# Performance work log

Measured on AMD Instinct MI355X. Metric: run time of the kernel, lower is better.

## Reference

```python
import jax, jax.numpy as jnp
import numpy as np

VOCAB = 6; C_IN = 4; D = 256; L = 4; T = 4096; B = 2
EXPAND = 2; DI = EXPAND * D  # 512
DS = 16; DCONV = 4; DTR = 16  # dt_rank = ceil(D/16)


def setup_inputs() -> dict:
    key = jax.random.key(0)
    ks = jax.random.split(key, 16)
    rn = lambda k, shape, s=0.02: jax.random.normal(k, shape, jnp.float32) * s
    return {
        "seq": jax.random.randint(ks[0], (B, T), 0, VOCAB),
        "input": jax.random.normal(ks[1], (B, T, C_IN), jnp.float32),
        "emb_table": rn(ks[2], (VOCAB, D)),
        "inproj_w": rn(ks[3], (D, C_IN)),
        "inproj_b": jnp.zeros((D,), jnp.float32),
        "blk_in_w": rn(ks[4], (L, 2 * DI, D)),
        "blk_in_b": jnp.zeros((L, 2 * DI), jnp.float32),
        "conv_w": rn(ks[5], (L, DI, DCONV), 0.1),
        "conv_b": jnp.zeros((L, DI), jnp.float32),
        "xproj_w": rn(ks[6], (L, DTR + 2 * DS, DI)),
        "dt_w": rn(ks[7], (L, DI, DTR), 0.1),
        "dt_b": rn(ks[8], (L, DI), 0.1),
        "A_log": jnp.log(jnp.broadcast_to(jnp.arange(1, DS + 1, dtype=jnp.float32), (L, DI, DS))),
        "Dp": jnp.ones((L, DI), jnp.float32),
        "blk_out_w": rn(ks[9], (L, D, DI)),
        "blk_out_b": jnp.zeros((L, D), jnp.float32),
        "ln_g": jnp.ones((L, D), jnp.float32),
        "ln_b": jnp.zeros((L, D), jnp.float32),
        "head_w": rn(ks[10], (VOCAB, D)),
        "head_b": jnp.zeros((VOCAB,), jnp.float32),
        "outp_w": rn(ks[11], (C_IN, D)),
        "outp_b": jnp.zeros((C_IN,), jnp.float32),
    }


def _layernorm(x, g, b):
    mu = x.mean(-1, keepdims=True)
    var = ((x - mu) ** 2).mean(-1, keepdims=True)
    return (x - mu) * jax.lax.rsqrt(var + 1e-5) * g + b


def _mamba(x, in_w, in_b, cw, cb, xpw, dtw, dtb, alog, dparam, ow, ob):
    # x: (B, T, D). Standard mamba-ssm Mamba block (d_state=DS, d_conv=DCONV, expand=2).
    Bsz = x.shape[0]
    xz = x @ in_w.T + in_b                      # (B, T, 2*DI)
    xs, z = jnp.split(xz, 2, axis=-1)           # each (B, T, DI)
    # causal depthwise conv1d over time
    xt = jnp.pad(xs.transpose(0, 2, 1), ((0, 0), (0, 0), (DCONV - 1, 0)))  # (B, DI, T+3)
    xc = jax.lax.conv_general_dilated(xt, cw[:, None, :], (1,), 'VALID',
                                      feature_group_count=DI)             # (B, DI, T)
    xc = jax.nn.silu(xc + cb[None, :, None]).transpose(0, 2, 1)           # (B, T, DI)
    # input-dependent dt, B, C
    x_dbl = xc @ xpw.T                          # (B, T, DTR+2*DS)
    dt, Bm, Cm = jnp.split(x_dbl, [DTR, DTR + DS], axis=-1)
    dt = jax.nn.softplus(dt @ dtw.T + dtb)      # (B, T, DI)
    A = -jnp.exp(alog)                          # (DI, DS)
    dA = jnp.exp(dt[..., None] * A)                                  # (B, T, DI, DS)
    dBx = dt[..., None] * Bm[:, :, None, :] * xc[..., None]          # (B, T, DI, DS)

    def step(h, ins):
        dA_t, dBx_t, C_t = ins                  # (B,DI,DS), (B,DI,DS), (B,DS)
        h = dA_t * h + dBx_t
        return h, jnp.einsum('bds,bs->bd', h, C_t)

    h0 = jnp.zeros((Bsz, DI, DS), xc.dtype)
    _, ys = jax.lax.scan(step, h0, (dA.transpose(1, 0, 2, 3),
                                    dBx.transpose(1, 0, 2, 3),
                                    Cm.transpose(1, 0, 2)))
    y = ys.transpose(1, 0, 2) + dparam * xc     # (B, T, DI)
    y = y * jax.nn.silu(z)
    return y @ ow.T + ob                        # (B, T, D)


def reference(seq, input, emb_table, inproj_w, inproj_b, blk_in_w, blk_in_b,
              conv_w, conv_b, xproj_w, dt_w, dt_b, A_log, Dp,
              blk_out_w, blk_out_b, ln_g, ln_b, head_w, head_b, outp_w, outp_b):
    x = emb_table[seq] + input @ inproj_w.T + inproj_b   # (B, T, D)
    for l in range(L):
        mx = _mamba(x, blk_in_w[l], blk_in_b[l], conv_w[l], conv_b[l],
                    xproj_w[l], dt_w[l], dt_b[l], A_log[l], Dp[l],
                    blk_out_w[l], blk_out_b[l])
        x = _layernorm(x + mx, ln_g[l], ln_b[l])
    return (x @ head_w.T + head_b, x @ outp_w.T + outp_b)
```

## Files before the change

### kernel.cpp

```cpp
#include <hip/hip_runtime.h>

typedef unsigned short u16;
typedef unsigned int u32;
typedef short bf16x8 __attribute__((ext_vector_type(8)));
typedef float f32x4 __attribute__((ext_vector_type(4)));

#define Tlen 4096
#define NTOK 8192
#define NCH  128
#define CH   32

enum : int {
  OFF_EMB     = 16,
  OFF_INPUT   = OFF_EMB + 1536,
  OFF_INPROJW = OFF_INPUT + 32768,
  OFF_INPROJB = OFF_INPROJW + 1024,
  OFF_BLKINW  = OFF_INPROJB + 256,
  OFF_BLKINB  = OFF_BLKINW + 1048576,
  OFF_CONVW   = OFF_BLKINB + 4096,
  OFF_CONVB   = OFF_CONVW + 8192,
  OFF_XPROJW  = OFF_CONVB + 2048,
  OFF_DTW     = OFF_XPROJW + 98304,
  OFF_DTB     = OFF_DTW + 32768,
  OFF_A       = OFF_DTB + 2048,
  OFF_DP      = OFF_A + 32768,
  OFF_BLKOUTW = OFF_DP + 2048,
  OFF_BLKOUTB = OFF_BLKOUTW + 524288,
  OFF_LNG     = OFF_BLKOUTB + 1024,
  OFF_LNB     = OFF_LNG + 1024,
  OFF_HEADW   = OFF_LNB + 1024,
  OFF_HEADB   = OFF_HEADW + 1536,
  OFF_OUTPW   = OFF_HEADB + 16,
  OFF_OUTPB   = OFF_OUTPW + 1024,
  OFF_X       = OFF_OUTPB + 16,
  OFF_DT      = OFF_X + NTOK*256,
  OFF_SD      = OFF_DT + NTOK*512,
  OFF_BM      = OFF_SD + 131072,
  OFF_CM      = OFF_BM + 131072,
  OFF_XSBL    = OFF_CM + 131072,
  OFF_Z16     = OFF_XSBL + NTOK*256,
  OFF_XC16    = OFF_Z16 + NTOK*256,
  OFF_X16     = OFF_XC16 + NTOK*256,
  OFF_WIN16   = OFF_X16 + NTOK*128,
  OFF_WOUT16  = OFF_WIN16 + 524288,
  OFF_BXD16   = OFF_WOUT16 + 262144,
  OFF_TOT     = OFF_BXD16 + 557056,
};

__device__ inline float bf2f(u16 u) { return __uint_as_float(((u32)u) << 16); }
__device__ inline u16 f2bf(float f) {
  u32 x = __float_as_uint(f);
  u32 r = x + 0x7fffu + ((x >> 16) & 1u);
  return (u16)(r >> 16);
}

__global__ void k_sentinel(u32* dout, int nw) {
  int i = blockIdx.x * blockDim.x + threadIdx.x;
  if (i < nw) dout[i] = 0x46404640u;
}

__global__ void k_detect(const u16* emb, int n, int* flag) {
  __shared__ int bad;
  if (threadIdx.x == 0) bad = 0;
  __syncthreads();
  int local = 0;
  for (int i = threadIdx.x; i < n; i += blockDim.x) {
    float v = bf2f(emb[i]);
    if (!(fabsf(v) < 100.0f)) local = 1;
  }
  if (local) atomicOr(&bad, 1);
  __syncthreads();
  if (threadIdx.x == 0) flag[0] = bad ? 0 : 1;
}

struct Seg { const void* src; int n; int off; int op; };
struct ConvArgs { Seg seg[21]; int nseg; };

__global__ void k_convert(ConvArgs a, float* ws, const int* flag) {
  int isb = *flag;
  for (int sgi = 0; sgi < a.nseg; sgi++) {
    Seg sg = a.seg[sgi];
    for (int i = blockIdx.x * blockDim.x + threadIdx.x; i < sg.n;
         i += gridDim.x * blockDim.x) {
      float v;
      if (isb) v = bf2f(((const u16*)sg.src)[i]);
      else     v = ((const float*)sg.src)[i];
      if (sg.op) v = -__expf(v);
      ws[sg.off + i] = v;
    }
  }
}

__global__ void k_w16(float* ws) {
  u16* win = (u16*)(ws + OFF_WIN16);
  u16* wout = (u16*)(ws + OFF_WOUT16);
  for (int i = blockIdx.x * blockDim.x + threadIdx.x; i < 1048576 + 524288;
       i += gridDim.x * blockDim.x) {
    if (i < 1048576) win[i] = f2bf(ws[OFF_BLKINW + i]);
    else             wout[i - 1048576] = f2bf(ws[OFF_BLKOUTW + i - 1048576]);
  }
}

__global__ void k_weff(float* ws) {
  u16* bxd = (u16*)(ws + OFF_BXD16);
  const int NXD = 4 * 544 * 512;
  for (int idx = blockIdx.x * blockDim.x + threadIdx.x; idx < NXD;
       idx += gridDim.x * blockDim.x) {
    int l = idx / (544 * 512);
    int rem = idx - l * (544 * 512);
    int row = rem >> 9, k = rem & 511;
    const float* xpw = ws + OFF_XPROJW + l * 24576;
    float v;
    if (row < 32) {
      v = xpw[(16 + row) * 512 + k];
    } else {
      const float* dtw = ws + OFF_DTW + l * 8192 + (row - 32) * 16;
      v = 0.f;
      #pragma unroll
      for (int r = 0; r < 16; r++) v += dtw[r] * xpw[r * 512 + k];
    }
    bxd[idx] = f2bf(v);
  }
}

__global__ __launch_bounds__(256) void k_embed(const int* seq, float* ws) {
  int n = blockIdx.x, d = threadIdx.x;
  int s = seq[n];
  float4 iv = *(const float4*)(ws + OFF_INPUT + n * 4);
  float4 wv = *(const float4*)(ws + OFF_INPROJW + d * 4);
  float acc = ws[OFF_EMB + s * 256 + d] + ws[OFF_INPROJB + d]
            + iv.x * wv.x + iv.y * wv.y + iv.z * wv.z + iv.w * wv.w;
  ws[OFF_X + (size_t)n * 256 + d] = acc;
  ((u16*)(ws + OFF_X16))[(size_t)n * 256 + d] = f2bf(acc);
}

__global__ __launch_bounds__(256) void k_gemm_in(float* ws, int l) {
  __shared__ u16 As[128][40];
  __shared__ u16 Bs[128][40];
  __shared__ u16 ot[64][136];
  int m0 = blockIdx.x * 128, n0g = blockIdx.y * 128;
  int t = threadIdx.x;
  int w = t >> 6, lane = t & 63;
  int fr = lane & 15, fq = lane >> 4;
  int wr = (w >> 1) * 64, wc = (w & 1) * 64;
  const u16* Ab = (const u16*)(ws + OFF_X16);
  const u16* Bb = (const u16*)(ws + OFF_WIN16) + (size_t)l * 1024 * 256;
  const float* bias = ws + OFF_BLKINB + l * 1024;
  f32x4 acc[4][4] = {};
  for (int k0 = 0; k0 < 256; k0 += 32) {
    __syncthreads();
    #pragma unroll
    for (int cc = 0; cc < 2; cc++) {
      int c = t + cc * 256;
      int row = c >> 2, cg = (c & 3) * 8;
      *(uint4*)&As[row][cg] =
          *(const uint4*)(Ab + (size_t)(m0 + row) * 256 + k0 + cg);
      *(uint4*)&Bs[row][cg] =
          *(const uint4*)(Bb + (size_t)(n0g + row) * 256 + k0 + cg);
    }
    __syncthreads();
    bf16x8 af[4], bf_[4];
    #pragma unroll
    for (int f = 0; f < 4; f++) {
      af[f]  = *(const bf16x8*)&As[wr + f * 16 + fr][fq * 8];
      bf_[f] = *(const bf16x8*)&Bs[wc + f * 16 + fr][fq * 8];
    }
    #pragma unroll
    for (int i = 0; i < 4; i++)
      #pragma unroll
      for (int j = 0; j < 4; j++)
        acc[i][j] = __builtin_amdgcn_mfma_f32_16x16x32_bf16(af[i], bf_[j],
                                                            acc[i][j], 0, 0, 0);
  }
  u16* plane; int cb0;
  if (n0g < 512) { plane = (u16*)(ws + OFF_XSBL); cb0 = n0g; }
  else           { plane = (u16*)(ws + OFF_Z16);  cb0 = n0g - 512; }
  #pragma unroll
  for (int hh = 0; hh < 2; hh++) {
    __syncthreads();
    if ((w >> 1) == hh) {
      #pragma unroll
      for (int i = 0; i < 4; i++)
        #pragma unroll
        for (int j = 0; j < 4; j++) {
          int col = wc + j * 16 + fr;
          float bv = bias[n0g + col];
          #pragma unroll
          for (int r = 0; r < 4; r++)
            ot[i * 16 + fq * 4 + r][col] = f2bf(acc[i][j][r] + bv);
        }
    }
    __syncthreads();
    int row = t >> 2, c0 = (t & 3) * 32;
    uint4 q0 = *(const uint4*)&ot[row][c0];
    uint4 q1 = *(const uint4*)&ot[row][c0 + 8];
    uint4 q2 = *(const uint4*)&ot[row][c0 + 16];
    uint4 q3 = *(const uint4*)&ot[row][c0 + 24];
    u16* dst = plane + (size_t)(m0 + hh * 64 + row) * 512 + cb0 + c0;
    *(uint4*)(dst + 0) = q0;
    *(uint4*)(dst + 8) = q1;
    *(uint4*)(dst + 16) = q2;
    *(uint4*)(dst + 24) = q3;
  }
}

__global__ __launch_bounds__(512) void k_conv(float* ws, int l) {
  int n0 = blockIdx.x * 16;
  int d = threadIdx.x;
  const float* cw = ws + OFF_CONVW + l * 2048;
  float4 w4 = *(const float4*)(cw + d * 4);
  float cbv = ws[OFF_CONVB + l * 512 + d];
  const u16* xs16 = (const u16*)(ws + OFF_XSBL);
  u16* xc16 = (u16*)(ws + OFF_XC16);
  float xm3, xm2, xm1;
  if ((n0 & (Tlen - 1)) == 0) {
    xm3 = xm2 = xm1 = 0.f;
  } else {
    xm3 = bf2f(xs16[(size_t)(n0 - 3) * 512 + d]);
    xm2 = bf2f(xs16[(size_t)(n0 - 2) * 512 + d]);
    xm1 = bf2f(xs16[(size_t)(n0 - 1) * 512 + d]);
  }
  #pragma unroll
  for (int tok = 0; tok < 16; tok++) {
    int n = n0 + tok;
    float xc = bf2f(xs16[(size_t)n * 512 + d]);
    float acc = cbv + xm3 * w4.x + xm2 * w4.y + xm1 * w4.z + xc * w4.w;
    float sv = acc / (1.f + __expf(-acc));
    xc16[(size_t)n * 512 + d] = f2bf(sv);
    xm3 = xm2; xm2 = xm1; xm1 = xc;
  }
}

__global__ __launch_bounds__(256) void k_gemm_xd(float* ws, int l) {
  __shared__ u16 dts[64][136];
  int by = blockIdx.y;
  int m0 = blockIdx.x * 64;
  int w = threadIdx.x >> 6, lane = threadIdx.x & 63;
  const u16* Ab = (const u16*)(ws + OFF_XC16);
  const u16* Bb = (const u16*)(ws + OFF_BXD16) + (size_t)l * 544 * 512;
  int ak = (lane >> 4) * 8;
  const u16* ap = Ab + (size_t)(m0 + w * 16 + (lane & 15)) * 512 + ak;
  int rowbase = w * 16 + (lane >> 4) * 4;
  if (by < 8) {
    const u16* bp = Bb + (size_t)(32 + by * 64 + (lane & 15)) * 512 + ak;
    f32x4 acc[4] = {};
    bf16x8 a0 = *(const bf16x8*)ap;
    bf16x8 b0[4];
    #pragma unroll
    for (int j = 0; j < 4; j++) b0[j] = *(const bf16x8*)(bp + (size_t)j * 8192);
    #pragma unroll 2
    for (int k0 = 1; k0 < 16; k0++) {
      bf16x8 a1 = *(const bf16x8*)(ap + k0 * 32);
      bf16x8 b1[4];
      #pragma unroll
      for (int j = 0; j < 4; j++)
        b1[j] = *(const bf16x8*)(bp + (size_t)j * 8192 + k0 * 32);
      #pragma unroll
      for (int j = 0; j < 4; j++)
        acc[j] = __builtin_amdgcn_mfma_f32_16x16x32_bf16(a0, b0[j], acc[j], 0, 0, 0);
      a0 = a1;
      #pragma unroll
      for (int j = 0; j < 4; j++) b0[j] = b1[j];
    }
    #pragma unroll
    for (int j = 0; j < 4; j++)
      acc[j] = __builtin_amdgcn_mfma_f32_16x16x32_bf16(a0, b0[j], acc[j], 0, 0, 0);
    const float* dtb = ws + OFF_DTB + l * 512;
    #pragma unroll
    for (int j = 0; j < 4; j++) {
      float bv = dtb[by * 64 + j * 16 + (lane & 15)];
      #pragma unroll
      for (int r = 0; r < 4; r++) {
        float s = acc[j][r] + bv;
        float dtv = (s > 20.f) ? s : log1pf(__expf(s));
        dts[rowbase + r][j * 16 + (lane & 15)] = f2bf(dtv);
      }
    }
    __syncthreads();
    u16* dt16 = (u16*)(ws + OFF_DT);
    int tt = threadIdx.x;
    int row = tt >> 2, part = tt & 3;
    uint4 v0 = *(const uint4*)&dts[row][part * 16];
    uint4 v1 = *(const uint4*)&dts[row][part * 16 + 8];
    u16* dst = dt16 + (size_t)(m0 + row) * 512 + by * 64 + part * 16;
    *(uint4*)dst = v0;
    *(uint4*)(dst + 8) = v1;
  } else {
    const u16* bp = Bb + (size_t)(lane & 15) * 512 + ak;
    f32x4 acc[2] = {};
    bf16x8 a0 = *(const bf16x8*)ap;
    bf16x8 b0[2];
    #pragma unroll
    for (int j = 0; j < 2; j++) b0[j] = *(const bf16x8*)(bp + (size_t)j * 8192);
    #pragma unroll 2
    for (int k0 = 1; k0 < 16; k0++) {
      bf16x8 a1 = *(const bf16x8*)(ap + k0 * 32);
      bf16x8 b1[2];
      #pragma unroll
      for (int j = 0; j < 2; j++)
        b1[j] = *(const bf16x8*)(bp + (size_t)j * 8192 + k0 * 32);
      #pragma unroll
      for (int j = 0; j < 2; j++)
        acc[j] = __builtin_amdgcn_mfma_f32_16x16x32_bf16(a0, b0[j], acc[j], 0, 0, 0);
      a0 = a1;
      #pragma unroll
      for (int j = 0; j < 2; j++) b0[j] = b1[j];
    }
    #pragma unroll
    for (int j = 0; j < 2; j++)
      acc[j] = __builtin_amdgcn_mfma_f32_16x16x32_bf16(a0, b0[j], acc[j], 0, 0, 0);
    int c = lane & 15;
    #pragma unroll
    for (int r = 0; r < 4; r++) {
      ws[OFF_BM + (size_t)(m0 + rowbase + r) * 16 + c] = acc[0][r];
      ws[OFF_CM + (size_t)(m0 + rowbase + r) * 16 + c] = acc[1][r];
    }
  }
}

__global__ __launch_bounds__(512) void k_scan1(float* ws, int l) {
  __shared__ u16 dt_s[8][512];
  __shared__ u16 xc_s[8][512];
  __shared__ float Bls[CH * 16];
  int blk = blockIdx.x;
  int b = blk >> 7, ch = blk & 127;
  int d = threadIdx.x;
  int nbase = b * Tlen + ch * CH;
  Bls[d] = ws[OFF_BM + (size_t)nbase * 16 + d];
  const float* Ap = ws + OFF_A + l * 8192 + d * 16;
  float Ar[16];
  *(float4*)&Ar[0]  = *(const float4*)(Ap + 0);
  *(float4*)&Ar[4]  = *(const float4*)(Ap + 4);
  *(float4*)&Ar[8]  = *(const float4*)(Ap + 8);
  *(float4*)&Ar[12] = *(const float4*)(Ap + 12);
  float h[16];
  #pragma unroll
  for (int s = 0; s < 16; s++) h[s] = 0.f;
  float sumdt = 0.f;
  const u16* dtg = (const u16*)(ws + OFF_DT) + (size_t)nbase * 512;
  const u16* xcg = (const u16*)(ws + OFF_XC16) + (size_t)nbase * 512;
  int lr = d >> 6, lc = (d & 63) * 8;
  uint4 pd = *(const uint4*)(dtg + (size_t)lr * 512 + lc);
  uint4 px = *(const uint4*)(xcg + (size_t)lr * 512 + lc);
  for (int st = 0; st < 4; st++) {
    *(uint4*)&dt_s[lr][lc] = pd;
    *(uint4*)&xc_s[lr][lc] = px;
    if (st < 3) {
      pd = *(const uint4*)(dtg + (size_t)(st * 8 + 8 + lr) * 512 + lc);
      px = *(const uint4*)(xcg + (size_t)(st * 8 + 8 + lr) * 512 + lc);
    }
    __syncthreads();
    #pragma unroll
    for (int tk = 0; tk < 8; tk++) {
      int tt = st * 8 + tk;
      float dtv = bf2f(dt_s[tk][d]);
      float xv = bf2f(xc_s[tk][d]);
      sumdt += dtv;
      float dtx = dtv * xv;
      #pragma unroll
      for (int s = 0; s < 16; s++)
        h[s] = __expf(dtv * Ar[s]) * h[s] + dtx * Bls[tt * 16 + s];
    }
    __syncthreads();
  }
  ws[OFF_SD + (size_t)blk * 512 + d] = sumdt;
  float* bl = ws + OFF_XSBL + ((size_t)blk * 512 + d) * 16;
  *(float4*)(bl + 0)  = make_float4(h[0], h[1], h[2], h[3]);
  *(float4*)(bl + 4)  = make_float4(h[4], h[5], h[6], h[7]);
  *(float4*)(bl + 8)  = make_float4(h[8], h[9], h[10], h[11]);
  *(float4*)(bl + 12) = make_float4(h[12], h[13], h[14], h[15]);
}

__global__ __launch_bounds__(256) void k_scan2(float* ws, int l) {
  int q = blockIdx.x * 256 + threadIdx.x;
  int b = q >> 13, ds = q & 8191, d = ds >> 4;
  float Av = ws[OFF_A + l * 8192 + ds];
  float* blhs = ws + OFF_XSBL;
  const float* sdp = ws + OFF_SD;
  size_t base = (size_t)(b * NCH) * 8192 + ds;
  size_t sbase = (size_t)(b * NCH) * 512 + d;
  float blv[4], sd[4];
  #pragma unroll
  for (int k = 0; k < 4; k++) {
    blv[k] = blhs[base + (size_t)k * 8192];
    sd[k] = sdp[sbase + (size_t)k * 512];
  }
  float h = 0.f;
  for (int g = 0; g < 32; g++) {
    float nblv[4], nsd[4];
    if (g < 31) {
      #pragma unroll
      for (int k = 0; k < 4; k++) {
        nblv[k] = blhs[base + (size_t)(g * 4 + 4 + k) * 8192];
        nsd[k] = sdp[sbase + (size_t)(g * 4 + 4 + k) * 512];
      }
    }
    #pragma unroll
    for (int k = 0; k < 4; k++) {
      blhs[base + (size_t)(g * 4 + k) * 8192] = h;
      h = __expf(sd[k] * Av) * h + blv[k];
    }
    #pragma unroll
    for (int k = 0; k < 4; k++) { blv[k] = nblv[k]; sd[k] = nsd[k]; }
  }
}

__global__ __launch_bounds__(512) void k_scan3(float* ws, int l) {
  __shared__ u16 dt_s[8][512];
  __shared__ u16 xc_s[8][512];
  __shared__ u16 z_s[8][512];
  __shared__ u16 y_s[8][512];
  __shared__ float Bls[CH * 16];
  __shared__ float Cls[CH * 16];
  int blk = blockIdx.x;
  int b = blk >> 7, ch = blk & 127;
  int d = threadIdx.x;
  int nbase = b * Tlen + ch * CH;
  Bls[d] = ws[OFF_BM + (size_t)nbase * 16 + d];
  Cls[d] = ws[OFF_CM + (size_t)nbase * 16 + d];
  const float* Ap = ws + OFF_A + l * 8192 + d * 16;
  float Ar[16];
  *(float4*)&Ar[0]  = *(const float4*)(Ap + 0);
  *(float4*)&Ar[4]  = *(const float4*)(Ap + 4);
  *(float4*)&Ar[8]  = *(const float4*)(Ap + 8);
  *(float4*)&Ar[12] = *(const float4*)(Ap + 12);
  float Dv = ws[OFF_DP + l * 512 + d];
  const float* hs = ws + OFF_XSBL + ((size_t)blk * 512 + d) * 16;
  float h[16];
  *(float4*)&h[0]  = *(const float4*)(hs + 0);
  *(float4*)&h[4]  = *(const float4*)(hs + 4);
  *(float4*)&h[8]  = *(const float4*)(hs + 8);
  *(float4*)&h[12] = *(const float4*)(hs + 12);
  const u16* dtg = (const u16*)(ws + OFF_DT) + (size_t)nbase * 512;
  u16* xcg = (u16*)(ws + OFF_XC16) + (size_t)nbase * 512;
  const u16* zg = (const u16*)(ws + OFF_Z16) + (size_t)nbase * 512;
  int lr = d >> 6, lc = (d & 63) * 8;
  size_t off0 = (size_t)lr * 512 + lc;
  uint4 pd = *(const uint4*)(dtg + off0);
  uint4 px = *(const uint4*)(xcg + off0);
  uint4 pz = *(const uint4*)(zg + off0);
  for (int st = 0; st < 4; st++) {
    size_t goff = (size_t)(st * 8 + lr) * 512 + lc;
    *(uint4*)&dt_s[lr][lc] = pd;
    *(uint4*)&xc_s[lr][lc] = px;
    *(uint4*)&z_s[lr][lc]  = pz;
    if (st < 3) {
      size_t noff = (size_t)(st * 8 + 8 + lr) * 512 + lc;
      pd = *(const uint4*)(dtg + noff);
      px = *(const uint4*)(xcg + noff);
      pz = *(const uint4*)(zg + noff);
    }
    __syncthreads();
    #pragma unroll
    for (int tk = 0; tk < 8; tk++) {
      int tt = st * 8 + tk;
      float dtv = bf2f(dt_s[tk][d]);
      float xv = bf2f(xc_s[tk][d]);
      float dtx = dtv * xv;
      float yacc = 0.f;
      #pragma unroll
      for (int s = 0; s < 16; s++) {
        h[s] = __expf(dtv * Ar[s]) * h[s] + dtx * Bls[tt * 16 + s];
        yacc += h[s] * Cls[tt * 16 + s];
      }
      float yv = yacc + Dv * xv;
      float zv = bf2f(z_s[tk][d]);
      float sz = zv / (1.f + __expf(-zv));
      y_s[tk][d] = f2bf(yv * sz);
    }
    __syncthreads();
    *(uint4*)(xcg + goff) = *(const uint4*)&y_s[lr][lc];
  }
}

__global__ __launch_bounds__(256) void k_gemm_out(float* ws, int l) {
  __shared__ float mxs[16][260];
  int m0 = blockIdx.x * 16;
  int w = threadIdx.x >> 6, lane = threadIdx.x & 63;
  const u16* Ab = (const u16*)(ws + OFF_XC16);
  const u16* Bb = (const u16*)(ws + OFF_WOUT16) + (size_t)l * 256 * 512;
  int ak = (lane >> 4) * 8;
  const u16* ap = Ab + (size_t)(m0 + (lane & 15)) * 512 + ak;
  const u16* bp = Bb + (size_t)(w * 64 + (lane & 15)) * 512 + ak;
  f32x4 acc[4] = {};
  bf16x8 a0 = *(const bf16x8*)ap;
  bf16x8 b0[4];
  #pragma unroll
  for (int j = 0; j < 4; j++) b0[j] = *(const bf16x8*)(bp + (size_t)j * 8192);
  #pragma unroll 2
  for (int k0 = 1; k0 < 16; k0++) {
    bf16x8 a1 = *(const bf16x8*)(ap + k0 * 32);
    bf16x8 b1[4];
    #pragma unroll
    for (int j = 0; j < 4; j++)
      b1[j] = *(const bf16x8*)(bp + (size_t)j * 8192 + k0 * 32);
    #pragma unroll
    for (int j = 0; j < 4; j++)
      acc[j] = __builtin_amdgcn_mfma_f32_16x16x32_bf16(a0, b0[j], acc[j], 0, 0, 0);
    a0 = a1;
    #pragma unroll
    for (int j = 0; j < 4; j++) b0[j] = b1[j];
  }
  #pragma unroll
  for (int j = 0; j < 4; j++)
    acc[j] = __builtin_amdgcn_mfma_f32_16x16x32_bf16(a0, b0[j], acc[j], 0, 0, 0);
  const float* ob = ws + OFF_BLKOUTB + l * 256;
  int rl = (lane >> 4) * 4;
  #pragma unroll
  for (int j = 0; j < 4; j++) {
    int c = w * 64 + j * 16 + (lane & 15);
    float bv = ob[c];
    #pragma unroll
    for (int r = 0; r < 4; r++)
      mxs[rl + r][c] = acc[j][r] + bv;
  }
  __syncthreads();
  int t = threadIdx.x;
  int g = t >> 4, ln = t & 15;
  int n = m0 + g;
  float* x = ws + OFF_X;
  const float* gamma = ws + OFF_LNG + l * 256;
  const float* beta = ws + OFF_LNB + l * 256;
  float v[16], s1 = 0.f, s2 = 0.f;
  #pragma unroll
  for (int i = 0; i < 16; i++) {
    int c = ln + i * 16;
    float xv = x[(size_t)n * 256 + c] + mxs[g][c];
    v[i] = xv; s1 += xv; s2 += xv * xv;
  }
  #pragma unroll
  for (int m = 8; m >= 1; m >>= 1) {
    s1 += __shfl_xor(s1, m, 64);
    s2 += __shfl_xor(s2, m, 64);
  }
  float mu = s1 * (1.f / 256.f);
  float var = s2 * (1.f / 256.f) - mu * mu;
  float rs = rsqrtf(var + 1e-5f);
  #pragma unroll
  for (int i = 0; i < 16; i++) {
    int c = ln + i * 16;
    mxs[g][c] = (v[i] - mu) * rs * gamma[c] + beta[c];
  }
  __syncthreads();
  int row = t >> 4, cb = (t & 15) * 16;
  float4 f0 = *(const float4*)&mxs[row][cb + 0];
  float4 f1 = *(const float4*)&mxs[row][cb + 4];
  float4 f2 = *(const float4*)&mxs[row][cb + 8];
  float4 f3 = *(const float4*)&mxs[row][cb + 12];
  float* xd = x + (size_t)(m0 + row) * 256 + cb;
  *(float4*)(xd + 0) = f0;
  *(float4*)(xd + 4) = f1;
  *(float4*)(xd + 8) = f2;
  *(float4*)(xd + 12) = f3;
  u32 p[8];
  p[0] = (u32)f2bf(f0.x) | ((u32)f2bf(f0.y) << 16);
  p[1] = (u32)f2bf(f0.z) | ((u32)f2bf(f0.w) << 16);
  p[2] = (u32)f2bf(f1.x) | ((u32)f2bf(f1.y) << 16);
  p[3] = (u32)f2bf(f1.z) | ((u32)f2bf(f1.w) << 16);
  p[4] = (u32)f2bf(f2.x) | ((u32)f2bf(f2.y) << 16);
  p[5] = (u32)f2bf(f2.z) | ((u32)f2bf(f2.w) << 16);
  p[6] = (u32)f2bf(f3.x) | ((u32)f2bf(f3.y) << 16);
  p[7] = (u32)f2bf(f3.z) | ((u32)f2bf(f3.w) << 16);
  u16* xd16 = (u16*)(ws + OFF_X16) + (size_t)(m0 + row) * 256 + cb;
  *(uint4*)(xd16 + 0) = *(uint4*)&p[0];
  *(uint4*)(xd16 + 8) = *(uint4*)&p[4];
}

__global__ __launch_bounds__(256) void k_head(const float* ws, void* dout,
                                              const int* flag) {
  int t = threadIdx.x;
  int lane = t & 63, w = t >> 6;
  int n = blockIdx.x * 4 + w;
  const float* xr = ws + OFF_X + (size_t)n * 256;
  float xv[4];
  #pragma unroll
  for (int i = 0; i < 4; i++) xv[i] = xr[lane + 64 * i];
  float res[10];
  #pragma unroll
  for (int o = 0; o < 10; o++) {
    const float* wr = (o < 6) ? ws + OFF_HEADW + o * 256
                              : ws + OFF_OUTPW + (o - 6) * 256;
    float p = 0.f;
    #pragma unroll
    for (int i = 0; i < 4; i++) p += xv[i] * wr[lane + 64 * i];
    #pragma unroll
    for (int m = 32; m >= 1; m >>= 1) p += __shfl_xor(p, m, 64);
    res[o] = p;
  }
  int isb = flag[0];
  if (lane < 6) {
    float vv = res[lane] + ws[OFF_HEADB + lane];
    size_t idx = (size_t)n * 6 + lane;
    if (isb) ((u16*)dout)[idx] = f2bf(vv);
    else     ((float*)dout)[idx] = vv;
  } else if (lane < 10) {
    int o = lane - 6;
    float vv = res[lane] + ws[OFF_OUTPB + o];
    size_t idx = (size_t)NTOK * 6 + (size_t)n * 4 + o;
    if (isb) ((u16*)dout)[idx] = f2bf(vv);
    else     ((float*)dout)[idx] = vv;
  }
}

extern "C" void kernel_launch(void* const* d_in, const int* in_sizes, int n_in,
                              void* d_out, int out_size, void* d_ws, size_t ws_size,
                              hipStream_t stream) {
  (void)n_in;
  float* ws = (float*)d_ws;
  int* flag = (int*)d_ws;

  if (ws_size < (size_t)OFF_TOT * 4) {
    int nw = out_size / 2;
    k_sentinel<<<(nw + 255) / 256, 256, 0, stream>>>((u32*)d_out, nw);
    return;
  }

  k_detect<<<1, 256, 0, stream>>>((const u16*)d_in[2], in_sizes[2], flag);

  ConvArgs ca;
  int i = 0;
  auto add = [&](int idx, int n, int off, int op) {
    ca.seg[i].src = d_in[idx]; ca.seg[i].n = n;
    ca.seg[i].off = off; ca.seg[i].op = op; i++;
  };
  add(2, 1536, OFF_EMB, 0);      add(1, 32768, OFF_INPUT, 0);
  add(3, 1024, OFF_INPROJW, 0);  add(4, 256, OFF_INPROJB, 0);
  add(5, 1048576, OFF_BLKINW, 0); add(6, 4096, OFF_BLKINB, 0);
  add(7, 8192, OFF_CONVW, 0);    add(8, 2048, OFF_CONVB, 0);
  add(9, 98304, OFF_XPROJW, 0);  add(10, 32768, OFF_DTW, 0);
  add(11, 2048, OFF_DTB, 0);     add(12, 32768, OFF_A, 1);
  add(13, 2048, OFF_DP, 0);      add(14, 524288, OFF_BLKOUTW, 0);
  add(15, 1024, OFF_BLKOUTB, 0); add(16, 1024, OFF_LNG, 0);
  add(17, 1024, OFF_LNB, 0);     add(18, 1536, OFF_HEADW, 0);
  add(19, 6, OFF_HEADB, 0);      add(20, 1024, OFF_OUTPW, 0);
  add(21, 4, OFF_OUTPB, 0);
  ca.nseg = i;
  k_convert<<<512, 256, 0, stream>>>(ca, ws, flag);
  k_w16<<<512, 256, 0, stream>>>(ws);
  k_weff<<<1024, 256, 0, stream>>>(ws);

  k_embed<<<NTOK, 256, 0, stream>>>((const int*)d_in[0], ws);

  for (int l = 0; l < 4; l++) {
    k_gemm_in<<<dim3(64, 8), 256, 0, stream>>>(ws, l);
    k_conv<<<NTOK / 16, 512, 0, stream>>>(ws, l);
    k_gemm_xd<<<dim3(128, 9), 256, 0, stream>>>(ws, l);
    k_scan1<<<2 * NCH, 512, 0, stream>>>(ws, l);
    k_scan2<<<64, 256, 0, stream>>>(ws, l);
    k_scan3<<<2 * NCH, 512, 0, stream>>>(ws, l);
    k_gemm_out<<<NTOK / 16, 256, 0, stream>>>(ws, l);
  }

  k_head<<<NTOK / 4, 256, 0, stream>>>(ws, d_out, flag);
}
```

Before: 639.7 us.

## Split fused x_proj/dt_proj GEMM into low-rank projection plus dt expansion kernel

Instead of precomputing the effective 512x512 dt weight (dt_w @ x_proj_dt) and running a K=512 GEMM with 544 output columns, the xc activations are now projected only onto 48 columns (B, C and the 16-wide dt rank). A separate kernel then expands the 16-rank dt to 512 channels with FMA and applies softplus. This cuts the MFMA work and the weight reads for the x-projection by roughly an order of magnitude. The cost is an extra kernel launch per layer, an extra fp32 intermediate round-trip through global memory, and a change in rounding because the dt expansion is now done in fp32 rather than through a bf16 effective weight.

```diff
diff --git a/kernel.cpp b/kernel.cpp
--- a/kernel.cpp
+++ b/kernel.cpp
@@ -44,7 +44,8 @@
   OFF_WIN16   = OFF_X16 + NTOK*128,
   OFF_WOUT16  = OFF_WIN16 + 524288,
   OFF_BXD16   = OFF_WOUT16 + 262144,
-  OFF_TOT     = OFF_BXD16 + 557056,
+  OFF_T       = OFF_BXD16 + 49152,
+  OFF_TOT     = OFF_T + 131072,
 };
 
 __device__ inline float bf2f(u16 u) { return __uint_as_float(((u32)u) << 16); }
@@ -101,24 +102,16 @@
   }
 }
 
-__global__ void k_weff(float* ws) {
+__global__ void k_bxd(float* ws) {
   u16* bxd = (u16*)(ws + OFF_BXD16);
-  const int NXD = 4 * 544 * 512;
+  const int NXD = 4 * 48 * 512;
   for (int idx = blockIdx.x * blockDim.x + threadIdx.x; idx < NXD;
        idx += gridDim.x * blockDim.x) {
-    int l = idx / (544 * 512);
-    int rem = idx - l * (544 * 512);
+    int l = idx / (48 * 512);
+    int rem = idx - l * (48 * 512);
     int row = rem >> 9, k = rem & 511;
     const float* xpw = ws + OFF_XPROJW + l * 24576;
-    float v;
-    if (row < 32) {
-      v = xpw[(16 + row) * 512 + k];
-    } else {
-      const float* dtw = ws + OFF_DTW + l * 8192 + (row - 32) * 16;
-      v = 0.f;
-      #pragma unroll
-      for (int r = 0; r < 16; r++) v += dtw[r] * xpw[r * 512 + k];
-    }
+    float v = (row < 32) ? xpw[(16 + row) * 512 + k] : xpw[(row - 32) * 512 + k];
     bxd[idx] = f2bf(v);
   }
 }
@@ -231,90 +224,75 @@
   }
 }
 
-__global__ __launch_bounds__(256) void k_gemm_xd(float* ws, int l) {
-  __shared__ u16 dts[64][136];
-  int by = blockIdx.y;
+__global__ __launch_bounds__(256) void k_gemm_bct(float* ws, int l) {
   int m0 = blockIdx.x * 64;
   int w = threadIdx.x >> 6, lane = threadIdx.x & 63;
   const u16* Ab = (const u16*)(ws + OFF_XC16);
-  const u16* Bb = (const u16*)(ws + OFF_BXD16) + (size_t)l * 544 * 512;
+  const u16* Bb = (const u16*)(ws + OFF_BXD16) + (size_t)l * 48 * 512;
   int ak = (lane >> 4) * 8;
   const u16* ap = Ab + (size_t)(m0 + w * 16 + (lane & 15)) * 512 + ak;
   int rowbase = w * 16 + (lane >> 4) * 4;
-  if (by < 8) {
-    const u16* bp = Bb + (size_t)(32 + by * 64 + (lane & 15)) * 512 + ak;
-    f32x4 acc[4] = {};
-    bf16x8 a0 = *(const bf16x8*)ap;
-    bf16x8 b0[4];
-    #pragma unroll
-    for (int j = 0; j < 4; j++) b0[j] = *(const bf16x8*)(bp + (size_t)j * 8192);
-    #pragma unroll 2
-    for (int k0 = 1; k0 < 16; k0++) {
-      bf16x8 a1 = *(const bf16x8*)(ap + k0 * 32);
-      bf16x8 b1[4];
-      #pragma unroll
-      for (int j = 0; j < 4; j++)
-        b1[j] = *(const bf16x8*)(bp + (size_t)j * 8192 + k0 * 32);
-      #pragma unroll
-      for (int j = 0; j < 4; j++)
-        acc[j] = __builtin_amdgcn_mfma_f32_16x16x32_bf16(a0, b0[j], acc[j], 0, 0, 0);
-      a0 = a1;
-      #pragma unroll
-      for (int j = 0; j < 4; j++) b0[j] = b1[j];
-    }
-    #pragma unroll
-    for (int j = 0; j < 4; j++)
+  const u16* bp = Bb + (size_t)(lane & 15) * 512 + ak;
+  f32x4 acc[3] = {};
+  bf16x8 a0 = *(const bf16x8*)ap;
+  bf16x8 b0[3];
+  #pragma unroll
+  for (int j = 0; j < 3; j++) b0[j] = *(const bf16x8*)(bp + (size_t)j * 8192);
+  #pragma unroll 2
+  for (int k0 = 1; k0 < 16; k0++) {
+    bf16x8 a1 = *(const bf16x8*)(ap + k0 * 32);
+    bf16x8 b1[3];
+    #pragma unroll
+    for (int j = 0; j < 3; j++)
+      b1[j] = *(const bf16x8*)(bp + (size_t)j * 8192 + k0 * 32);
+    #pragma unroll
+    for (int j = 0; j < 3; j++)
       acc[j] = __builtin_amdgcn_mfma_f32_16x16x32_bf16(a0, b0[j], acc[j], 0, 0, 0);
-    const float* dtb = ws + OFF_DTB + l * 512;
-    #pragma unroll
-    for (int j = 0; j < 4; j++) {
-      float bv = dtb[by * 64 + j * 16 + (lane & 15)];
-      #pragma unroll
-      for (int r = 0; r < 4; r++) {
-        float s = acc[j][r] + bv;
-        float dtv = (s > 20.f) ? s : log1pf(__expf(s));
-        dts[rowbase + r][j * 16 + (lane & 15)] = f2bf(dtv);
-      }
-    }
-    __syncthreads();
-    u16* dt16 = (u16*)(ws + OFF_DT);
-    int tt = threadIdx.x;
-    int row = tt >> 2, part = tt & 3;
-    uint4 v0 = *(const uint4*)&dts[row][part * 16];
-    uint4 v1 = *(const uint4*)&dts[row][part * 16 + 8];
-    u16* dst = dt16 + (size_t)(m0 + row) * 512 + by * 64 + part * 16;
-    *(uint4*)dst = v0;
-    *(uint4*)(dst + 8) = v1;
-  } else {
-    const u16* bp = Bb + (size_t)(lane & 15) * 512 + ak;
-    f32x4 acc[2] = {};
-    bf16x8 a0 = *(const bf16x8*)ap;
-    bf16x8 b0[2];
-    #pragma unroll
-    for (int j = 0; j < 2; j++) b0[j] = *(const bf16x8*)(bp + (size_t)j * 8192);
-    #pragma unroll 2
-    for (int k0 = 1; k0 < 16; k0++) {
-      bf16x8 a1 = *(const bf16x8*)(ap + k0 * 32);
-      bf16x8 b1[2];
-      #pragma unroll
-      for (int j = 0; j < 2; j++)
-        b1[j] = *(const bf16x8*)(bp + (size_t)j * 8192 + k0 * 32);
-      #pragma unroll
-      for (int j = 0; j < 2; j++)
-        acc[j] = __builtin_amdgcn_mfma_f32_16x16x32_bf16(a0, b0[j], acc[j], 0, 0, 0);
-      a0 = a1;
-      #pragma unroll
-      for (int j = 0; j < 2; j++) b0[j] = b1[j];
-    }
-    #pragma unroll
-    for (int j = 0; j < 2; j++)
-      acc[j] = __builtin_amdgcn_mfma_f32_16x16x32_bf16(a0, b0[j], acc[j], 0, 0, 0);
-    int c = lane & 15;
-    #pragma unroll
-    for (int r = 0; r < 4; r++) {
-      ws[OFF_BM + (size_t)(m0 + rowbase + r) * 16 + c] = acc[0][r];
-      ws[OFF_CM + (size_t)(m0 + rowbase + r) * 16 + c] = acc[1][r];
-    }
+    a0 = a1;
+    #pragma unroll
+    for (int j = 0; j < 3; j++) b0[j] = b1[j];
+  }
+  #pragma unroll
+  for (int j = 0; j < 3; j++)
+    acc[j] = __builtin_amdgcn_mfma_f32_16x16x32_bf16(a0, b0[j], acc[j], 0, 0, 0);
+  int c = lane & 15;
+  #pragma unroll
+  for (int r = 0; r < 4; r++) {
+    ws[OFF_BM + (size_t)(m0 + rowbase + r) * 16 + c] = acc[0][r];
+    ws[OFF_CM + (size_t)(m0 + rowbase + r) * 16 + c] = acc[1][r];
+    ws[OFF_T  + (size_t)(m0 + rowbase + r) * 16 + c] = acc[2][r];
+  }
+}
+
+__global__ __launch_bounds__(256) void k_dtexp(float* ws, int l) {
+  __shared__ float Ts[16][16];
+  int n0 = blockIdx.x * 16;
+  int t = threadIdx.x;
+  Ts[t >> 4][t & 15] = ws[OFF_T + (size_t)n0 * 16 + t];
+  const float* dtwp = ws + OFF_DTW + (size_t)l * 8192;
+  float w0[16], w1[16];
+  #pragma unroll
+  for (int q = 0; q < 4; q++) {
+    *(float4*)&w0[q * 4] = *(const float4*)(dtwp + (2 * t) * 16 + q * 4);
+    *(float4*)&w1[q * 4] = *(const float4*)(dtwp + (2 * t + 1) * 16 + q * 4);
+  }
+  float b0 = ws[OFF_DTB + l * 512 + 2 * t];
+  float b1 = ws[OFF_DTB + l * 512 + 2 * t + 1];
+  __syncthreads();
+  u16* dt16 = (u16*)(ws + OFF_DT);
+  #pragma unroll
+  for (int tok = 0; tok < 16; tok++) {
+    float s0 = b0, s1 = b1;
+    #pragma unroll
+    for (int r = 0; r < 16; r++) {
+      float tv = Ts[tok][r];
+      s0 += tv * w0[r];
+      s1 += tv * w1[r];
+    }
+    float d0 = (s0 > 20.f) ? s0 : log1pf(__expf(s0));
+    float d1 = (s1 > 20.f) ? s1 : log1pf(__expf(s1));
+    *(u32*)(dt16 + (size_t)(n0 + tok) * 512 + 2 * t) =
+        (u32)f2bf(d0) | ((u32)f2bf(d1) << 16);
   }
 }
 
@@ -637,14 +615,15 @@
   ca.nseg = i;
   k_convert<<<512, 256, 0, stream>>>(ca, ws, flag);
   k_w16<<<512, 256, 0, stream>>>(ws);
-  k_weff<<<1024, 256, 0, stream>>>(ws);
+  k_bxd<<<384, 256, 0, stream>>>(ws);
 
   k_embed<<<NTOK, 256, 0, stream>>>((const int*)d_in[0], ws);
 
   for (int l = 0; l < 4; l++) {
     k_gemm_in<<<dim3(64, 8), 256, 0, stream>>>(ws, l);
     k_conv<<<NTOK / 16, 512, 0, stream>>>(ws, l);
-    k_gemm_xd<<<dim3(128, 9), 256, 0, stream>>>(ws, l);
+    k_gemm_bct<<<128, 256, 0, stream>>>(ws, l);
+    k_dtexp<<<NTOK / 16, 256, 0, stream>>>(ws, l);
     k_scan1<<<2 * NCH, 512, 0, stream>>>(ws, l);
     k_scan2<<<64, 256, 0, stream>>>(ws, l);
     k_scan3<<<2 * NCH, 512, 0, stream>>>(ws, l);
```

New measurement: 562.2 us. -12.1%, faster.
